# Kernel optimization log

Hardware: AMD Instinct MI355X
Metric: run time of the kernel (lower is better)

## Reference

```python
import jax, jax.numpy as jnp
import numpy as np

MIN_DELAY = 60
MAX_DELAY = 420
TAU = 0.0          # module's self.tau (min magnitude for resonant_activation)
TEMPERATURE = 1.0  # forward() default gumbel-softmax temperature


def setup_inputs() -> dict:
    key = jax.random.key(0)
    k1, k2, k3, k4 = jax.random.split(key, 4)
    B, T = 128, 8192
    excitation = jax.random.normal(k1, (B, 1, T), dtype=jnp.float32)
    u = jax.random.uniform(k2, (MAX_DELAY - MIN_DELAY,), dtype=jnp.float32,
                           minval=1e-6, maxval=1.0 - 1e-6)
    gumbel_noise = -jnp.log(-jnp.log(u))  # standard Gumbel samples
    delay_param = jax.random.normal(k3, (MAX_DELAY - MIN_DELAY,), dtype=jnp.float32)
    feedback_gain = jnp.ones((1,), dtype=jnp.float32)
    reflection_coeffs = jax.random.normal(k4, (2,), dtype=jnp.float32)
    return {"excitation": excitation, "gumbel_noise": gumbel_noise,
            "delay_param": delay_param, "feedback_gain": feedback_gain,
            "reflection_coeffs": reflection_coeffs}


def _resonant_activation(x, min_magnitude):
    sign = jnp.sign(x)
    magnitude = jnp.abs(jnp.tanh(x))
    return sign * (min_magnitude + (1.0 - min_magnitude) * magnitude)


def _build_coeffs(gumbel_noise, delay_param, feedback_gain, reflection_coeffs):
    # gumbel_softmax(tau=TEMPERATURE, hard=True) with straight-through estimator
    logits = (delay_param + gumbel_noise) / TEMPERATURE
    soft = jax.nn.softmax(logits)
    hard = jax.nn.one_hot(jnp.argmax(soft), soft.shape[0], dtype=soft.dtype)
    one_hot = jax.lax.stop_gradient(hard - soft) + soft
    shifted = jnp.roll(one_hot, 1)
    # low_pass_bias=False -> tanh, then resonant_activation (applies tanh again, as in source)
    rc = jnp.tanh(reflection_coeffs)
    k1 = _resonant_activation(rc[0], TAU)
    k2 = _resonant_activation(rc[1], TAU)
    a1 = k1 * (1.0 - k2)
    a2 = jnp.clip(k2, -0.999, 0.999)
    a1_bound = 0.999 - jnp.abs(a2)
    a1 = jnp.clip(a1, -a1_bound, a1_bound)
    g = jax.nn.sigmoid(feedback_gain[0]) ** 0.45
    a1 = a1 * g
    a2 = a2 * g
    tail = one_hot * a1 + shifted * a2               # [max_delay - min_delay]
    coeffs = jnp.concatenate([jnp.zeros((MIN_DELAY,), tail.dtype), tail])  # [max_delay]
    return coeffs


def _sample_wise_lpc(x, coeffs):
    # All-pole IIR: y[t] = x[t] - sum_{i=0}^{D-1} coeffs[i] * y[t-1-i]
    B, T = x.shape
    D = coeffs.shape[0]
    buf0 = jnp.zeros((B, D), x.dtype)  # buf[:, i] = y[t-1-i]

    def step(buf, x_t):
        y_t = x_t - buf @ coeffs                              # [B]
        buf = jnp.concatenate([y_t[:, None], buf[:, :-1]], 1)  # shift delay line
        return buf, y_t

    _, ys = jax.lax.scan(step, buf0, x.T)  # ys: [T, B]
    return ys.T


def reference(excitation, gumbel_noise, delay_param, feedback_gain, reflection_coeffs):
    coeffs = _build_coeffs(gumbel_noise, delay_param, feedback_gain, reflection_coeffs)
    x = excitation[:, 0, :]                 # [B, T]
    y = _sample_wise_lpc(x, coeffs)         # [B, T]
    return y[:, None, :]                    # [B, 1, T]
```

## Files before the change

kernel.cpp:

```cpp
#include <hip/hip_runtime.h>
#include <cmath>

#define T_LEN 8192
#define B_ROWS 128
#define ND 360
#define MIN_DELAY_C 60
#define BLOCK 512

__global__ __launch_bounds__(BLOCK) void ks_resonator_kernel(
    const float* __restrict__ excitation,
    const float* __restrict__ gumbel,
    const float* __restrict__ delay_param,
    const float* __restrict__ feedback_gain,
    const float* __restrict__ refl,
    float* __restrict__ out)
{
    __shared__ float y[T_LEN];
    __shared__ float red_v[BLOCK];
    __shared__ int   red_i[BLOCK];
    __shared__ float s_a1, s_a2;
    __shared__ int   s_lagA, s_lagB;

    const int tid = threadIdx.x;
    const int row = blockIdx.x;

    float v = -INFINITY; int idx = 0;
    if (tid < ND) { v = delay_param[tid] + gumbel[tid]; idx = tid; }
    red_v[tid] = v; red_i[tid] = idx;
    __syncthreads();
    for (int off = BLOCK / 2; off > 0; off >>= 1) {
        if (tid < off) {
            float v2 = red_v[tid + off]; int i2 = red_i[tid + off];
            float v1 = red_v[tid];       int i1 = red_i[tid];
            if (v2 > v1 || (v2 == v1 && i2 < i1)) { red_v[tid] = v2; red_i[tid] = i2; }
        }
        __syncthreads();
    }

    if (tid == 0) {
        int p = red_i[0];
        float k1 = tanhf(tanhf(refl[0]));
        float k2 = tanhf(tanhf(refl[1]));
        float a1 = k1 * (1.0f - k2);
        float a2 = fminf(fmaxf(k2, -0.999f), 0.999f);
        float bound = 0.999f - fabsf(a2);
        a1 = fminf(fmaxf(a1, -bound), bound);
        float fg = feedback_gain[0];
        float g = powf(1.0f / (1.0f + expf(-fg)), 0.45f);
        a1 *= g; a2 *= g;
        int p2 = (p + 1) % ND;
        s_a1 = a1; s_a2 = a2;
        s_lagA = MIN_DELAY_C + p + 1;
        s_lagB = MIN_DELAY_C + p2 + 1;
    }
    __syncthreads();

    const float a1 = s_a1, a2 = s_a2;
    const int lagA = s_lagA, lagB = s_lagB;
    const int C = (lagA < lagB) ? lagA : lagB;

    const float* x = excitation + (size_t)row * T_LEN;
    for (int i = tid; i < T_LEN; i += BLOCK) y[i] = x[i];
    __syncthreads();

    for (int pos = 0; pos < T_LEN; pos += C) {
        int end = pos + C; if (end > T_LEN) end = T_LEN;
        for (int j = pos + tid; j < end; j += BLOCK) {
            float ya = (j >= lagA) ? y[j - lagA] : 0.0f;
            float yb = (j >= lagB) ? y[j - lagB] : 0.0f;
            y[j] = y[j] - a1 * ya - a2 * yb;
        }
        __syncthreads();
    }

    float* o = out + (size_t)row * T_LEN;
    for (int i = tid; i < T_LEN; i += BLOCK) o[i] = y[i];
}

extern "C" void kernel_launch(void* const* d_in, const int* in_sizes, int n_in,
                              void* d_out, int out_size, void* d_ws, size_t ws_size,
                              hipStream_t stream) {
    const float* excitation    = (const float*)d_in[0];
    const float* gumbel        = (const float*)d_in[1];
    const float* delay_param   = (const float*)d_in[2];
    const float* feedback_gain = (const float*)d_in[3];
    const float* refl          = (const float*)d_in[4];
    float* out = (float*)d_out;

    ks_resonator_kernel<<<B_ROWS, BLOCK, 0, stream>>>(
        excitation, gumbel, delay_param, feedback_gain, refl, out);
}
```

Before: 72.77 us.

## Use single-wavefront blocks to drop barriers and shuffle-reduce argmax

Launches one 64-lane wavefront per row instead of 512 threads, so the per-chunk block barriers in the recurrence loop can be removed and ordering relies on wavefront lockstep. The argmax over delay logits uses cross-lane shuffles instead of a shared-memory tree, and every lane computes the coefficients itself rather than broadcasting them through shared memory. Loads and stores use float4. The risk is less parallelism per row during the copy phases, and the code depends on wave64 execution semantics for correctness.

```diff
diff --git a/kernel.cpp b/kernel.cpp
--- a/kernel.cpp
+++ b/kernel.cpp
@@ -5,9 +5,8 @@
 #define B_ROWS 128
 #define ND 360
 #define MIN_DELAY_C 60
-#define BLOCK 512
 
-__global__ __launch_bounds__(BLOCK) void ks_resonator_kernel(
+__global__ __launch_bounds__(64) void ks_resonator_kernel(
     const float* __restrict__ excitation,
     const float* __restrict__ gumbel,
     const float* __restrict__ delay_param,
@@ -16,65 +15,56 @@
     float* __restrict__ out)
 {
     __shared__ float y[T_LEN];
-    __shared__ float red_v[BLOCK];
-    __shared__ int   red_i[BLOCK];
-    __shared__ float s_a1, s_a2;
-    __shared__ int   s_lagA, s_lagB;
 
-    const int tid = threadIdx.x;
-    const int row = blockIdx.x;
+    const int lane = threadIdx.x;
+    const int row  = blockIdx.x;
 
-    float v = -INFINITY; int idx = 0;
-    if (tid < ND) { v = delay_param[tid] + gumbel[tid]; idx = tid; }
-    red_v[tid] = v; red_i[tid] = idx;
-    __syncthreads();
-    for (int off = BLOCK / 2; off > 0; off >>= 1) {
-        if (tid < off) {
-            float v2 = red_v[tid + off]; int i2 = red_i[tid + off];
-            float v1 = red_v[tid];       int i1 = red_i[tid];
-            if (v2 > v1 || (v2 == v1 && i2 < i1)) { red_v[tid] = v2; red_i[tid] = i2; }
-        }
-        __syncthreads();
+    float best = -INFINITY;
+    int   bi   = 0;
+    for (int i = lane; i < ND; i += 64) {
+        float v = delay_param[i] + gumbel[i];
+        if (v > best) { best = v; bi = i; }
     }
+    #pragma unroll
+    for (int off = 32; off > 0; off >>= 1) {
+        float v2 = __shfl_xor(best, off);
+        int   i2 = __shfl_xor(bi, off);
+        if (v2 > best || (v2 == best && i2 < bi)) { best = v2; bi = i2; }
+    }
+    const int p = bi;
 
-    if (tid == 0) {
-        int p = red_i[0];
-        float k1 = tanhf(tanhf(refl[0]));
-        float k2 = tanhf(tanhf(refl[1]));
-        float a1 = k1 * (1.0f - k2);
-        float a2 = fminf(fmaxf(k2, -0.999f), 0.999f);
-        float bound = 0.999f - fabsf(a2);
-        a1 = fminf(fmaxf(a1, -bound), bound);
-        float fg = feedback_gain[0];
-        float g = powf(1.0f / (1.0f + expf(-fg)), 0.45f);
-        a1 *= g; a2 *= g;
-        int p2 = (p + 1) % ND;
-        s_a1 = a1; s_a2 = a2;
-        s_lagA = MIN_DELAY_C + p + 1;
-        s_lagB = MIN_DELAY_C + p2 + 1;
-    }
-    __syncthreads();
+    float k1 = tanhf(tanhf(refl[0]));
+    float k2 = tanhf(tanhf(refl[1]));
+    float a1 = k1 * (1.0f - k2);
+    float a2 = fminf(fmaxf(k2, -0.999f), 0.999f);
+    float bound = 0.999f - fabsf(a2);
+    a1 = fminf(fmaxf(a1, -bound), bound);
+    float g = powf(1.0f / (1.0f + expf(-feedback_gain[0])), 0.45f);
+    a1 *= g; a2 *= g;
 
-    const float a1 = s_a1, a2 = s_a2;
-    const int lagA = s_lagA, lagB = s_lagB;
-    const int C = (lagA < lagB) ? lagA : lagB;
+    const int lagA = MIN_DELAY_C + p + 1;
+    const int lagB = MIN_DELAY_C + ((p + 1) % ND) + 1;
+    const int C    = (lagA < lagB) ? lagA : lagB;
 
-    const float* x = excitation + (size_t)row * T_LEN;
-    for (int i = tid; i < T_LEN; i += BLOCK) y[i] = x[i];
-    __syncthreads();
+    const float4* xv = (const float4*)(excitation + (size_t)row * T_LEN);
+    float4*       yv = (float4*)y;
+    #pragma unroll 8
+    for (int i = 0; i < T_LEN / 4 / 64; i++)
+        yv[i * 64 + lane] = xv[i * 64 + lane];
 
     for (int pos = 0; pos < T_LEN; pos += C) {
         int end = pos + C; if (end > T_LEN) end = T_LEN;
-        for (int j = pos + tid; j < end; j += BLOCK) {
+        for (int j = pos + lane; j < end; j += 64) {
             float ya = (j >= lagA) ? y[j - lagA] : 0.0f;
             float yb = (j >= lagB) ? y[j - lagB] : 0.0f;
             y[j] = y[j] - a1 * ya - a2 * yb;
         }
-        __syncthreads();
     }
 
-    float* o = out + (size_t)row * T_LEN;
-    for (int i = tid; i < T_LEN; i += BLOCK) o[i] = y[i];
+    float4* ov = (float4*)(out + (size_t)row * T_LEN);
+    #pragma unroll 8
+    for (int i = 0; i < T_LEN / 4 / 64; i++)
+        ov[i * 64 + lane] = yv[i * 64 + lane];
 }
 
 extern "C" void kernel_launch(void* const* d_in, const int* in_sizes, int n_in,
@@ -87,6 +77,6 @@
     const float* refl          = (const float*)d_in[4];
     float* out = (float*)d_out;
 
-    ks_resonator_kernel<<<B_ROWS, BLOCK, 0, stream>>>(
+    ks_resonator_kernel<<<B_ROWS, 64, 0, stream>>>(
         excitation, gumbel, delay_param, feedback_gain, refl, out);
 }
```

Result: slower. 82.96 us (+14.0%).
